# Performance work log

Hardware: AMD Instinct MI355X
Metric: run time of the kernel (lower is better)

Reference implementation:

```python
import jax, jax.numpy as jnp
import numpy as np

N_NODES = 50000
N_EDGES = 800000
IN_F = 128
HEADS = 4
OUT_F = 32
NEG_SLOPE = 0.2


def setup_inputs() -> dict:
    key = jax.random.key(0)
    k1, k2, k3, k4 = jax.random.split(key, 4)
    x = jax.random.normal(k1, (1, N_NODES, IN_F), dtype=jnp.float32)
    edge_index = jax.random.randint(k2, (2, N_EDGES), 0, N_NODES, dtype=jnp.int64)
    # nn.Linear(in, heads*out, bias=False): weight shape [heads*out, in]
    W = jax.random.normal(k3, (HEADS * OUT_F, IN_F), dtype=jnp.float32) * 0.05
    att = jax.random.normal(k4, (1, HEADS, 2 * OUT_F), dtype=jnp.float32) * 0.05
    bias = jnp.zeros((HEADS * OUT_F,), dtype=jnp.float32)
    return {"x": x, "edge_index": edge_index, "W": W, "att": att, "bias": bias}


def reference(x, edge_index, W, att, bias):
    B, n, _ = x.shape
    # h = W(x) -> [B, N, H, F]
    h = (x @ W.T).reshape(B, n, HEADS, OUT_F)
    # add self loops
    loops = jnp.arange(n, dtype=edge_index.dtype)
    src = jnp.concatenate([edge_index[0], loops])
    dst = jnp.concatenate([edge_index[1], loops])
    # attention scores: leaky_relu(cat(h_src, h_dst)) . att  -> [B, Etot, H]
    h_cat = jnp.concatenate([h[:, src], h[:, dst]], axis=-1)  # [B, Etot, H, 2F]
    att_in = jax.nn.leaky_relu(h_cat, NEG_SLOPE)
    scores = jnp.sum(att_in * att, axis=-1)  # att [1,H,2F] broadcasts -> [B, Etot, H]
    # NOTE: faithful to the original: softmax over the FULL edge axis (dim=1),
    # not a per-destination segment softmax.
    w = jax.nn.softmax(scores, axis=1)  # [B, Etot, H]
    # aggregate: scatter-add weighted source features to destination nodes
    weighted = h[:, src] * w[..., None]  # [B, Etot, H, F]
    out = jax.vmap(lambda wf: jax.ops.segment_sum(wf, dst, num_segments=n))(weighted)
    # [B, N, H, F] -> [B, N, H*F] + bias
    return out.reshape(B, n, HEADS * OUT_F) + bias
```

## Files before the change

kernel.cpp:

```cpp
#include <hip/hip_runtime.h>
#include <math.h>

#define N_NODES 50000
#define N_EDGES 800000
#define E_TOT   850000
#define IN_F    128
#define HEADS   4
#define OUT_F   32
#define HF      128
#define NEG_SLOPE 0.2f
#define ELLW    40
#define OVF_CAP 4096
#define DEN_SLOTS 16

#define WS_G      0
#define WS_ES     6400000
#define WS_ED     6600000
#define WS_DEN    6800000
#define WS_CNT    6830000
#define WS_ELL    6880000
#define WS_OVFC   8880000
#define WS_OVFS   8880064
#define WS_OVFD   8884160
#define NBLK_EDGE 3321

static __device__ __forceinline__ float4 ld4(const float* p) {
    return *reinterpret_cast<const float4*>(p);
}

__global__ __launch_bounds__(256) void k_gemm_attprep(
    const float* __restrict__ x, const float* __restrict__ W,
    const float* __restrict__ att, float* __restrict__ g,
    float* __restrict__ es, float* __restrict__ ed,
    int* __restrict__ cnt, int* __restrict__ ovf_cnt,
    float* __restrict__ denom)
{
    __shared__ float wt[32 * 128];
    const int t  = threadIdx.x;
    const int n0 = blockIdx.x * 32;

    if (t < 32) {
        int z = n0 + t;
        if (z < N_NODES) cnt[z] = 0;
    }
    if (blockIdx.x == 0) {
        if (t == 0) *ovf_cnt = 0;
        if (t < DEN_SLOTS * 4) denom[t] = 0.f;
    }

    const int cg = t & 31;
    const int nr = t >> 5;
    float4 acc[4];
    #pragma unroll
    for (int ni = 0; ni < 4; ++ni) acc[ni] = make_float4(0.f, 0.f, 0.f, 0.f);

    const float4* wt4 = reinterpret_cast<const float4*>(wt);
    const float4* x4  = reinterpret_cast<const float4*>(x);

    int row[4];
    #pragma unroll
    for (int ni = 0; ni < 4; ++ni) {
        int n = n0 + nr + ni * 8;
        row[ni] = n < N_NODES ? n : N_NODES - 1;
    }

    for (int kt = 0; kt < 4; ++kt) {
        __syncthreads();
        {
            const int c = t >> 1, half = t & 1;
            #pragma unroll
            for (int i = 0; i < 4; ++i) {
                float4 wv = ld4(W + c * 128 + kt * 32 + half * 16 + i * 4);
                int kk = half * 16 + i * 4;
                wt[(kk + 0) * 128 + c] = wv.x;
                wt[(kk + 1) * 128 + c] = wv.y;
                wt[(kk + 2) * 128 + c] = wv.z;
                wt[(kk + 3) * 128 + c] = wv.w;
            }
        }
        __syncthreads();

        #pragma unroll
        for (int kk4 = 0; kk4 < 8; ++kk4) {
            float xv[4][4];
            #pragma unroll
            for (int ni = 0; ni < 4; ++ni)
                *reinterpret_cast<float4*>(xv[ni]) =
                    x4[row[ni] * 32 + kt * 8 + kk4];
            #pragma unroll
            for (int j = 0; j < 4; ++j) {
                float4 wv = wt4[(kk4 * 4 + j) * 32 + cg];
                #pragma unroll
                for (int ni = 0; ni < 4; ++ni) {
                    acc[ni].x += xv[ni][j] * wv.x;
                    acc[ni].y += xv[ni][j] * wv.y;
                    acc[ni].z += xv[ni][j] * wv.z;
                    acc[ni].w += xv[ni][j] * wv.w;
                }
            }
        }
    }

    const int head = cg >> 3;
    const int f0   = (cg & 7) * 4;
    float4 as = ld4(att + head * 64 + f0);
    float4 ad = ld4(att + head * 64 + 32 + f0);

    #pragma unroll
    for (int ni = 0; ni < 4; ++ni) {
        int n = n0 + nr + ni * 8;
        if (n < N_NODES) {
            float lx = acc[ni].x > 0.f ? acc[ni].x : NEG_SLOPE * acc[ni].x;
            float ly = acc[ni].y > 0.f ? acc[ni].y : NEG_SLOPE * acc[ni].y;
            float lz = acc[ni].z > 0.f ? acc[ni].z : NEG_SLOPE * acc[ni].z;
            float lw = acc[ni].w > 0.f ? acc[ni].w : NEG_SLOPE * acc[ni].w;
            float ps = lx * as.x + ly * as.y + lz * as.z + lw * as.w;
            float pd = lx * ad.x + ly * ad.y + lz * ad.z + lw * ad.w;
            ps += __shfl_xor(ps, 1); ps += __shfl_xor(ps, 2); ps += __shfl_xor(ps, 4);
            pd += __shfl_xor(pd, 1); pd += __shfl_xor(pd, 2); pd += __shfl_xor(pd, 4);
            float esv = expf(ps);
            float4 gv = make_float4(acc[ni].x * esv, acc[ni].y * esv,
                                    acc[ni].z * esv, acc[ni].w * esv);
            *reinterpret_cast<float4*>(&g[n * 128 + cg * 4]) = gv;
            if ((t & 7) == 0) {
                es[n * 4 + head] = esv;
                ed[n * 4 + head] = expf(pd);
            }
        }
    }
}

__global__ __launch_bounds__(256) void k_edge_fill_denom(
    const int* __restrict__ eidx, const float* __restrict__ es,
    const float* __restrict__ ed, int* __restrict__ cnt,
    int* __restrict__ ell, int* __restrict__ ovf_cnt,
    int* __restrict__ ovf_s, int* __restrict__ ovf_d,
    float* __restrict__ denom)
{
    __shared__ float4 red[256];
    const int t = threadIdx.x;
    const int e = blockIdx.x * 256 + t;
    float4 w = make_float4(0.f, 0.f, 0.f, 0.f);
    if (e < E_TOT) {
        int s, d;
        if (e < N_EDGES) {
            s = eidx[e]; d = eidx[N_EDGES + e];
            int pos = atomicAdd(&cnt[d], 1);
            if (pos < ELLW) {
                ell[d * ELLW + pos] = s;
            } else {
                int o = atomicAdd(ovf_cnt, 1);
                if (o < OVF_CAP) { ovf_s[o] = s; ovf_d[o] = d; }
            }
        } else {
            s = d = e - N_EDGES;
        }
        float4 vs = ld4(es + s * 4);
        float4 vd = ld4(ed + d * 4);
        w.x = vs.x * vd.x;
        w.y = vs.y * vd.y;
        w.z = vs.z * vd.z;
        w.w = vs.w * vd.w;
    }
    red[t] = w;
    __syncthreads();
    for (int sdt = 128; sdt > 0; sdt >>= 1) {
        if (t < sdt) {
            float4 o = red[t + sdt];
            red[t].x += o.x; red[t].y += o.y; red[t].z += o.z; red[t].w += o.w;
        }
        __syncthreads();
    }
    if (t < 4)
        atomicAdd(&denom[(blockIdx.x & (DEN_SLOTS - 1)) * 4 + t],
                  reinterpret_cast<const float*>(&red[0])[t]);
}

__global__ __launch_bounds__(256) void k_gather(
    const int* __restrict__ cnt, const int* __restrict__ ell,
    const float* __restrict__ ed, const float* __restrict__ g,
    const float* __restrict__ denom, const float* __restrict__ bias,
    const int* __restrict__ ovf_cnt, const int* __restrict__ ovf_s,
    const int* __restrict__ ovf_d, float* __restrict__ out)
{
    const int t = threadIdx.x;
    const int n = blockIdx.x * 8 + (t >> 5);
    if (n >= N_NODES) return;
    const int lane = t & 31;
    const int head = lane >> 3;

    float4 acc = ld4(g + n * 128 + lane * 4);

    const int raw = cnt[n];
    const int deg = min(raw, ELLW);
    const int* __restrict__ row = ell + n * ELLW;
    int j = 0;
    for (; j + 3 < deg; j += 4) {
        int s0 = row[j],     s1 = row[j + 1];
        int s2 = row[j + 2], s3 = row[j + 3];
        float4 g0 = ld4(g + s0 * 128 + lane * 4);
        float4 g1 = ld4(g + s1 * 128 + lane * 4);
        float4 g2 = ld4(g + s2 * 128 + lane * 4);
        float4 g3 = ld4(g + s3 * 128 + lane * 4);
        acc.x += g0.x + g1.x + g2.x + g3.x;
        acc.y += g0.y + g1.y + g2.y + g3.y;
        acc.z += g0.z + g1.z + g2.z + g3.z;
        acc.w += g0.w + g1.w + g2.w + g3.w;
    }
    for (; j < deg; ++j) {
        int s0 = row[j];
        float4 g0 = ld4(g + s0 * 128 + lane * 4);
        acc.x += g0.x; acc.y += g0.y; acc.z += g0.z; acc.w += g0.w;
    }

    if (raw > ELLW) {
        int m = min(*ovf_cnt, OVF_CAP);
        for (int i = 0; i < m; ++i) {
            if (ovf_d[i] == n) {
                int s = ovf_s[i];
                float4 g0 = ld4(g + s * 128 + lane * 4);
                acc.x += g0.x; acc.y += g0.y; acc.z += g0.z; acc.w += g0.w;
            }
        }
    }

    float dsum = 0.f;
    #pragma unroll
    for (int i2 = 0; i2 < DEN_SLOTS; ++i2) dsum += denom[i2 * 4 + head];

    const float sc = ed[n * 4 + head] / dsum;
    float4 b = ld4(bias + lane * 4);
    float4 o = make_float4(acc.x * sc + b.x, acc.y * sc + b.y,
                           acc.z * sc + b.z, acc.w * sc + b.w);
    *reinterpret_cast<float4*>(out + n * 128 + lane * 4) = o;
}

extern "C" void kernel_launch(void* const* d_in, const int* in_sizes, int n_in,
                              void* d_out, int out_size, void* d_ws, size_t ws_size,
                              hipStream_t stream) {
    const float* x    = (const float*)d_in[0];
    const int*   eidx = (const int*)d_in[1];
    const float* W    = (const float*)d_in[2];
    const float* att  = (const float*)d_in[3];
    const float* bias = (const float*)d_in[4];
    float* out = (float*)d_out;
    float* ws  = (float*)d_ws;

    float* g      = ws + WS_G;
    float* es     = ws + WS_ES;
    float* ed     = ws + WS_ED;
    float* denom  = ws + WS_DEN;
    int*   cnt    = (int*)(ws + WS_CNT);
    int*   ell    = (int*)(ws + WS_ELL);
    int*   ovfc   = (int*)(ws + WS_OVFC);
    int*   ovfs   = (int*)(ws + WS_OVFS);
    int*   ovfd   = (int*)(ws + WS_OVFD);

    k_gemm_attprep   <<<(N_NODES + 31) / 32, 256, 0, stream>>>(x, W, att, g, es, ed, cnt, ovfc, denom);
    k_edge_fill_denom<<<NBLK_EDGE,           256, 0, stream>>>(eidx, es, ed, cnt, ell, ovfc, ovfs, ovfd, denom);
    k_gather         <<<(N_NODES + 7) / 8,   256, 0, stream>>>(cnt, ell, ed, g, denom, bias, ovfc, ovfs, ovfd, out);
}
```

Before: 231.7 us.

## Store projected features in bf16, 16-bit ELL indices, XCD-partitioned edge fill

Projected per-node features g are now stored as bf16 rather than fp32, which halves the bytes read in the random-access gather. ELL neighbor indices are stored as 16-bit values instead of 32-bit. The edge-fill kernel is launched with eight times as many blocks, and each block handles only destinations in one node range, aiming to keep the atomics and ELL writes local to an XCD's L2; the denominator reduction runs only in the xcd==0 blocks. Risks: bf16 rounding lowers accuracy, 16-bit indices cannot hold node ids up to 50000 above 65535 (they fit here), and every edge-index read is repeated by eight blocks.

```diff
diff --git a/kernel.cpp b/kernel.cpp
--- a/kernel.cpp
+++ b/kernel.cpp
@@ -12,25 +12,37 @@
 #define ELLW    40
 #define OVF_CAP 4096
 #define DEN_SLOTS 16
+#define NXCD    8
+#define DPX     6250
 
 #define WS_G      0
-#define WS_ES     6400000
-#define WS_ED     6600000
-#define WS_DEN    6800000
-#define WS_CNT    6830000
-#define WS_ELL    6880000
-#define WS_OVFC   8880000
-#define WS_OVFS   8880064
-#define WS_OVFD   8884160
+#define WS_ES     3200000
+#define WS_ED     3400000
+#define WS_DEN    3600000
+#define WS_CNT    3610000
+#define WS_ELL    3660000
+#define WS_OVFC   4660000
+#define WS_OVFS   4660064
+#define WS_OVFD   4664160
 #define NBLK_EDGE 3321
 
 static __device__ __forceinline__ float4 ld4(const float* p) {
     return *reinterpret_cast<const float4*>(p);
 }
+static __device__ __forceinline__ unsigned short f2bf(float f) {
+    unsigned u = __float_as_uint(f);
+    return (unsigned short)((u + 0x7FFFu + ((u >> 16) & 1u)) >> 16);
+}
+static __device__ __forceinline__ float4 bf2f4(ushort4 v) {
+    return make_float4(__uint_as_float((unsigned)v.x << 16),
+                       __uint_as_float((unsigned)v.y << 16),
+                       __uint_as_float((unsigned)v.z << 16),
+                       __uint_as_float((unsigned)v.w << 16));
+}
 
 __global__ __launch_bounds__(256) void k_gemm_attprep(
     const float* __restrict__ x, const float* __restrict__ W,
-    const float* __restrict__ att, float* __restrict__ g,
+    const float* __restrict__ att, unsigned short* __restrict__ g,
     float* __restrict__ es, float* __restrict__ ed,
     int* __restrict__ cnt, int* __restrict__ ovf_cnt,
     float* __restrict__ denom)
@@ -119,9 +131,12 @@
             ps += __shfl_xor(ps, 1); ps += __shfl_xor(ps, 2); ps += __shfl_xor(ps, 4);
             pd += __shfl_xor(pd, 1); pd += __shfl_xor(pd, 2); pd += __shfl_xor(pd, 4);
             float esv = expf(ps);
-            float4 gv = make_float4(acc[ni].x * esv, acc[ni].y * esv,
-                                    acc[ni].z * esv, acc[ni].w * esv);
-            *reinterpret_cast<float4*>(&g[n * 128 + cg * 4]) = gv;
+            ushort4 sv;
+            sv.x = f2bf(acc[ni].x * esv);
+            sv.y = f2bf(acc[ni].y * esv);
+            sv.z = f2bf(acc[ni].z * esv);
+            sv.w = f2bf(acc[ni].w * esv);
+            *reinterpret_cast<ushort4*>(&g[n * 128 + cg * 4]) = sv;
             if ((t & 7) == 0) {
                 es[n * 4 + head] = esv;
                 ed[n * 4 + head] = expf(pd);
@@ -133,52 +148,61 @@
 __global__ __launch_bounds__(256) void k_edge_fill_denom(
     const int* __restrict__ eidx, const float* __restrict__ es,
     const float* __restrict__ ed, int* __restrict__ cnt,
-    int* __restrict__ ell, int* __restrict__ ovf_cnt,
+    unsigned short* __restrict__ ell, int* __restrict__ ovf_cnt,
     int* __restrict__ ovf_s, int* __restrict__ ovf_d,
     float* __restrict__ denom)
 {
     __shared__ float4 red[256];
-    const int t = threadIdx.x;
-    const int e = blockIdx.x * 256 + t;
-    float4 w = make_float4(0.f, 0.f, 0.f, 0.f);
-    if (e < E_TOT) {
-        int s, d;
-        if (e < N_EDGES) {
-            s = eidx[e]; d = eidx[N_EDGES + e];
+    const int t     = threadIdx.x;
+    const int chunk = blockIdx.x >> 3;
+    const int xcd   = blockIdx.x & 7;
+    const int e     = chunk * 256 + t;
+
+    if (e < N_EDGES) {
+        int d = eidx[N_EDGES + e];
+        if (d >= xcd * DPX && d < (xcd + 1) * DPX) {
+            int s = eidx[e];
             int pos = atomicAdd(&cnt[d], 1);
             if (pos < ELLW) {
-                ell[d * ELLW + pos] = s;
+                ell[d * ELLW + pos] = (unsigned short)s;
             } else {
                 int o = atomicAdd(ovf_cnt, 1);
                 if (o < OVF_CAP) { ovf_s[o] = s; ovf_d[o] = d; }
             }
-        } else {
-            s = d = e - N_EDGES;
-        }
-        float4 vs = ld4(es + s * 4);
-        float4 vd = ld4(ed + d * 4);
-        w.x = vs.x * vd.x;
-        w.y = vs.y * vd.y;
-        w.z = vs.z * vd.z;
-        w.w = vs.w * vd.w;
-    }
-    red[t] = w;
-    __syncthreads();
-    for (int sdt = 128; sdt > 0; sdt >>= 1) {
-        if (t < sdt) {
-            float4 o = red[t + sdt];
-            red[t].x += o.x; red[t].y += o.y; red[t].z += o.z; red[t].w += o.w;
-        }
+        }
+    }
+
+    if (xcd == 0) {
+        float4 w = make_float4(0.f, 0.f, 0.f, 0.f);
+        if (e < E_TOT) {
+            int s, d;
+            if (e < N_EDGES) { s = eidx[e]; d = eidx[N_EDGES + e]; }
+            else             { s = d = e - N_EDGES; }
+            float4 vs = ld4(es + s * 4);
+            float4 vd = ld4(ed + d * 4);
+            w.x = vs.x * vd.x;
+            w.y = vs.y * vd.y;
+            w.z = vs.z * vd.z;
+            w.w = vs.w * vd.w;
+        }
+        red[t] = w;
         __syncthreads();
-    }
-    if (t < 4)
-        atomicAdd(&denom[(blockIdx.x & (DEN_SLOTS - 1)) * 4 + t],
-                  reinterpret_cast<const float*>(&red[0])[t]);
+        for (int sdt = 128; sdt > 0; sdt >>= 1) {
+            if (t < sdt) {
+                float4 o = red[t + sdt];
+                red[t].x += o.x; red[t].y += o.y; red[t].z += o.z; red[t].w += o.w;
+            }
+            __syncthreads();
+        }
+        if (t < 4)
+            atomicAdd(&denom[(chunk & (DEN_SLOTS - 1)) * 4 + t],
+                      reinterpret_cast<const float*>(&red[0])[t]);
+    }
 }
 
 __global__ __launch_bounds__(256) void k_gather(
-    const int* __restrict__ cnt, const int* __restrict__ ell,
-    const float* __restrict__ ed, const float* __restrict__ g,
+    const int* __restrict__ cnt, const unsigned short* __restrict__ ell,
+    const float* __restrict__ ed, const unsigned short* __restrict__ g,
     const float* __restrict__ denom, const float* __restrict__ bias,
     const int* __restrict__ ovf_cnt, const int* __restrict__ ovf_s,
     const int* __restrict__ ovf_d, float* __restrict__ out)
@@ -189,19 +213,21 @@
     const int lane = t & 31;
     const int head = lane >> 3;
 
-    float4 acc = ld4(g + n * 128 + lane * 4);
+    const ushort4* g4 = reinterpret_cast<const ushort4*>(g);
+
+    float4 acc = bf2f4(g4[n * 32 + lane]);
 
     const int raw = cnt[n];
     const int deg = min(raw, ELLW);
-    const int* __restrict__ row = ell + n * ELLW;
+    const unsigned short* __restrict__ row = ell + n * ELLW;
     int j = 0;
     for (; j + 3 < deg; j += 4) {
         int s0 = row[j],     s1 = row[j + 1];
         int s2 = row[j + 2], s3 = row[j + 3];
-        float4 g0 = ld4(g + s0 * 128 + lane * 4);
-        float4 g1 = ld4(g + s1 * 128 + lane * 4);
-        float4 g2 = ld4(g + s2 * 128 + lane * 4);
-        float4 g3 = ld4(g + s3 * 128 + lane * 4);
+        float4 g0 = bf2f4(g4[s0 * 32 + lane]);
+        float4 g1 = bf2f4(g4[s1 * 32 + lane]);
+        float4 g2 = bf2f4(g4[s2 * 32 + lane]);
+        float4 g3 = bf2f4(g4[s3 * 32 + lane]);
         acc.x += g0.x + g1.x + g2.x + g3.x;
         acc.y += g0.y + g1.y + g2.y + g3.y;
         acc.z += g0.z + g1.z + g2.z + g3.z;
@@ -209,7 +235,7 @@
     }
     for (; j < deg; ++j) {
         int s0 = row[j];
-        float4 g0 = ld4(g + s0 * 128 + lane * 4);
+        float4 g0 = bf2f4(g4[s0 * 32 + lane]);
         acc.x += g0.x; acc.y += g0.y; acc.z += g0.z; acc.w += g0.w;
     }
 
@@ -217,8 +243,7 @@
         int m = min(*ovf_cnt, OVF_CAP);
         for (int i = 0; i < m; ++i) {
             if (ovf_d[i] == n) {
-                int s = ovf_s[i];
-                float4 g0 = ld4(g + s * 128 + lane * 4);
+                float4 g0 = bf2f4(g4[ovf_s[i] * 32 + lane]);
                 acc.x += g0.x; acc.y += g0.y; acc.z += g0.z; acc.w += g0.w;
             }
         }
@@ -246,17 +271,17 @@
     float* out = (float*)d_out;
     float* ws  = (float*)d_ws;
 
-    float* g      = ws + WS_G;
+    unsigned short* g   = (unsigned short*)(ws + WS_G);
     float* es     = ws + WS_ES;
     float* ed     = ws + WS_ED;
     float* denom  = ws + WS_DEN;
     int*   cnt    = (int*)(ws + WS_CNT);
-    int*   ell    = (int*)(ws + WS_ELL);
+    unsigned short* ell = (unsigned short*)(ws + WS_ELL);
     int*   ovfc   = (int*)(ws + WS_OVFC);
     int*   ovfs   = (int*)(ws + WS_OVFS);
     int*   ovfd   = (int*)(ws + WS_OVFD);
 
     k_gemm_attprep   <<<(N_NODES + 31) / 32, 256, 0, stream>>>(x, W, att, g, es, ed, cnt, ovfc, denom);
-    k_edge_fill_denom<<<NBLK_EDGE,           256, 0, stream>>>(eidx, es, ed, cnt, ell, ovfc, ovfs, ovfd, denom);
+    k_edge_fill_denom<<<NBLK_EDGE * NXCD,    256, 0, stream>>>(eidx, es, ed, cnt, ell, ovfc, ovfs, ovfd, denom);
     k_gather         <<<(N_NODES + 7) / 8,   256, 0, stream>>>(cnt, ell, ed, g, denom, bias, ovfc, ovfs, ovfd, out);
 }
```

New measurement: 228.6 us. No clear change (-1.4%).
